# Performance work log

Measured on AMD Instinct MI355X. Metric: run time of the kernel, lower is better.

Reference implementation:

```python
import jax, jax.numpy as jnp
import numpy as np

K = 40        # nearest neighbors
BN_EPS = 1e-5  # nn.BatchNorm1d default eps


def _bn(x, g, b):
    # training-mode BatchNorm1d: batch mean, biased variance
    mu = x.mean(0)
    var = x.var(0)
    return g * (x - mu) / jnp.sqrt(var + BN_EPS) + b


def setup_inputs() -> dict:
    key = jax.random.key(0)
    ks = jax.random.split(key, 16)
    N, Cin, D, S, P = 8192, 16, 32, 3, 32

    def w(k, i, o):
        return jax.random.normal(k, (i, o), jnp.float32) * (1.0 / np.sqrt(i))

    return {
        "x": jax.random.normal(ks[0], (N, Cin), jnp.float32),
        "original_coords": jax.random.normal(ks[1], (N, 3), jnp.float32),
        "batch": jnp.zeros((N,), jnp.int32),
        "step_count": 0,
        "num_layer": 1,
        # pre_gravnet MLP
        "pre_w1": w(ks[2], Cin, D), "pre_b1": jnp.zeros((D,), jnp.float32),
        "pre_w2": w(ks[3], D, D), "pre_b2": jnp.zeros((D,), jnp.float32),
        "bn1_g": jnp.ones((D,), jnp.float32), "bn1_b": jnp.zeros((D,), jnp.float32),
        # GravNetConv projections
        "lin_s_w": w(ks[4], D, S),
        "lin_h_w": w(ks[5], D, P), "lin_h_b": jnp.zeros((P,), jnp.float32),
        "lin_w": w(ks[6], D + 2 * P, D), "lin_b": jnp.zeros((D,), jnp.float32),
        # post_gravnet MLP (in = out_channels + space_dims + d_shape = 32+3+32)
        "post_w1": w(ks[7], D + S + D, D), "post_b1": jnp.zeros((D,), jnp.float32),
        "post_w2": w(ks[8], D, D), "post_b2": jnp.zeros((D,), jnp.float32),
        "bn2_g": jnp.ones((D,), jnp.float32), "bn2_b": jnp.zeros((D,), jnp.float32),
    }


def reference(x, original_coords, batch, step_count, num_layer,
              pre_w1, pre_b1, pre_w2, pre_b2, bn1_g, bn1_b,
              lin_s_w, lin_h_w, lin_h_b, lin_w, lin_b,
              post_w1, post_b1, post_w2, post_b2, bn2_g, bn2_b):
    N = x.shape[0]

    # pre_gravnet MLP + batchnorm
    h = jax.nn.elu(x @ pre_w1 + pre_b1)
    h = jax.nn.elu(h @ pre_w2 + pre_b2)
    x_in = _bn(h, bn1_g, bn1_b)

    # GravNetConv projections
    h_l = x_in @ lin_h_w + lin_h_b          # [N, P] propagated features
    s_l = x_in @ lin_s_w                    # [N, S] learned coordinate space

    # kNN graph in s-space (self loops excluded)
    sq = jnp.sum(s_l * s_l, axis=1)
    d2 = sq[:, None] + sq[None, :] - 2.0 * (s_l @ s_l.T)   # [N, N]
    d2 = jnp.maximum(d2, 0.0)
    d2 = jnp.where(jnp.eye(N, dtype=bool), jnp.inf, d2)
    _, idx = jax.lax.top_k(-d2, K)           # [N, K] neighbor indices

    # per-edge squared distance (NOTE: propagate uses the SQUARED distance,
    # faithful to the source where edge_weight is never re-bound to sqrt)
    edge_sq = jnp.take_along_axis(d2, idx, axis=1)    # [N, K]
    dist = jnp.sqrt(edge_sq + 1e-6)                   # [N, K]

    # DGL-side reductions at dst = edge_index[1] = neighbor index
    dst = idx.reshape(-1)
    distf = dist.reshape(-1)
    indeg = jax.ops.segment_sum(jnp.ones_like(distf), dst, num_segments=N)
    sum_d = jax.ops.segment_sum(distf, dst, num_segments=N)
    avdist = jnp.where(indeg > 0, sum_d / jnp.maximum(indeg, 1.0), 0.0)
    loss_regularizing_neig = 0.01 * jnp.mean(jnp.square(avdist - 0.5))

    norm_d = distf / (sum_d + 1e-4)[dst]              # EdgeWeightNorm('right')
    # faithful to source bug: '_edge_w_gndist' is set to the NORMALIZED dist,
    # and apply_edges multiplies by the RAW '_edge_w'
    degs2 = jax.ops.segment_sum(norm_d, dst, num_segments=N) + 1e-4
    gn_final = distf / degs2[dst]
    loss_llregulariser = 0.1 * jnp.mean(jnp.square(norm_d - gn_final))

    # message passing: msg = h_l[neighbor] * squared_dist, mean+max over the
    # K neighbors of each source node (regular fan-in -> dense reduce)
    msgs = h_l[idx] * edge_sq[..., None]              # [N, K, P]
    agg = jnp.concatenate([msgs.mean(1), msgs.max(1)], axis=-1)  # [N, 2P]
    xgn = jnp.concatenate([agg, x_in], axis=-1) @ lin_w + lin_b   # [N, 32]

    # post_gravnet MLP + batchnorm
    cat = jnp.concatenate([xgn, s_l, x_in], axis=1)   # [N, 67]
    o = jax.nn.elu(cat @ post_w1 + post_b1)
    o = jax.nn.elu(o @ post_w2 + post_b2)
    out = _bn(o, bn2_g, bn2_b)
    return (out, loss_regularizing_neig, loss_llregulariser)
```

## Files before the change

kernel.cpp:

```cpp
#include <hip/hip_runtime.h>
#include <math.h>

#define NPTS 8192
#define KNN 40
#define DD 32
#define CIN 16
#define RPB 8
#define CAP 96

#define OFF_H      0u
#define OFF_XIN    262144u
#define OFF_HL     524288u
#define OFF_SL     786432u
#define OFF_ESQ    819200u
#define OFF_O      1146880u
#define OFF_IDX    1409024u
#define OFF_SUMD   1736704u
#define OFF_INDEG  1744896u
#define OFF_STATS  1753088u
#define ZERO_FLOATS (8192u + 8192u + 130u * 32u)

#define ST(i) stats[(i) * 32]

__device__ __forceinline__ float elu_f(float x) { return x > 0.f ? x : (expf(x) - 1.f); }

__device__ __forceinline__ float grp_sum32(float v) {
#pragma unroll
    for (int m = 1; m < 32; m <<= 1) v += __shfl_xor(v, m);
    return v;
}

__device__ __forceinline__ unsigned fkey(float x) {
    unsigned b = __float_as_uint(x);
    return b ^ ((unsigned)((int)b >> 31) | 0x80000000u);
}
__device__ __forceinline__ float kinv(unsigned k) {
    unsigned b = (k & 0x80000000u) ? (k ^ 0x80000000u) : ~k;
    return __uint_as_float(b);
}

__device__ __forceinline__ unsigned bisect_kth(unsigned u0, unsigned u1, int kth) {
    unsigned lo = 0u, hi = 0xFFFFFFFFu;
    while (lo < hi) {
        unsigned mid = lo + ((hi - lo) >> 1);
        int cnt = __popcll(__ballot(u0 <= mid)) + __popcll(__ballot(u1 <= mid));
        if (cnt >= kth) hi = mid; else lo = mid + 1;
    }
    return hi;
}

__global__ __launch_bounds__(256) void k_pre(const float* __restrict__ x,
    const float* __restrict__ w1, const float* __restrict__ b1,
    const float* __restrict__ w2, const float* __restrict__ b2,
    float* __restrict__ h, float* __restrict__ stats)
{
    __shared__ float sw1[CIN * DD], sw2[DD * DD], sb1[DD], sb2[DD];
    __shared__ float bufx[RPB][20], buft[RPB][36];
    __shared__ float sstat[2 * DD];
    int tid = threadIdx.x;
    for (int t = tid; t < CIN * DD; t += 256) sw1[t] = w1[t];
    for (int t = tid; t < DD * DD; t += 256) sw2[t] = w2[t];
    if (tid < DD) { sb1[tid] = b1[tid]; sb2[tid] = b2[tid]; }
    if (tid < 2 * DD) sstat[tid] = 0.f;

    int r = tid >> 5, ch = tid & 31;
    int g = blockIdx.x * RPB + r;
    if (ch < CIN) bufx[r][ch] = x[(size_t)g * CIN + ch];
    __syncthreads();

    float acc = sb1[ch];
#pragma unroll
    for (int k4 = 0; k4 < CIN; k4 += 4) {
        float4 v = *(const float4*)&bufx[r][k4];
        acc = fmaf(v.x, sw1[(k4 + 0) * DD + ch], acc);
        acc = fmaf(v.y, sw1[(k4 + 1) * DD + ch], acc);
        acc = fmaf(v.z, sw1[(k4 + 2) * DD + ch], acc);
        acc = fmaf(v.w, sw1[(k4 + 3) * DD + ch], acc);
    }
    acc = elu_f(acc);
    buft[r][ch] = acc;
    __syncthreads();

    float o = sb2[ch];
#pragma unroll
    for (int k4 = 0; k4 < DD; k4 += 4) {
        float4 v = *(const float4*)&buft[r][k4];
        o = fmaf(v.x, sw2[(k4 + 0) * DD + ch], o);
        o = fmaf(v.y, sw2[(k4 + 1) * DD + ch], o);
        o = fmaf(v.z, sw2[(k4 + 2) * DD + ch], o);
        o = fmaf(v.w, sw2[(k4 + 3) * DD + ch], o);
    }
    o = elu_f(o);
    h[(size_t)g * DD + ch] = o;

    float s = o + __shfl_xor(o, 32);
    float q = o * o;
    q += __shfl_xor(q, 32);
    if ((tid & 32) == 0) { atomicAdd(&sstat[ch], s); atomicAdd(&sstat[DD + ch], q); }
    __syncthreads();
    if (tid < 2 * DD) atomicAdd(&ST(tid), sstat[tid]);
}

__global__ __launch_bounds__(256) void k_proj(const float* __restrict__ h,
    const float* __restrict__ stats,
    const float* __restrict__ g1, const float* __restrict__ b1g,
    const float* __restrict__ hw, const float* __restrict__ hb,
    const float* __restrict__ sw,
    float* __restrict__ xin, float* __restrict__ hl, float4* __restrict__ sl4)
{
    __shared__ float shw[DD * DD], ssw[DD * 3], sa[DD], sbp[DD], shb[DD];
    __shared__ float rrow[RPB][36];
    int tid = threadIdx.x;
    for (int t = tid; t < DD * DD; t += 256) shw[t] = hw[t];
    if (tid < DD * 3) ssw[tid] = sw[tid];
    if (tid < DD) {
        float mean = ST(tid) * (1.f / NPTS);
        float var = ST(32 + tid) * (1.f / NPTS) - mean * mean;
        float a = g1[tid] * rsqrtf(var + 1e-5f);
        sa[tid] = a;
        sbp[tid] = b1g[tid] - a * mean;
        shb[tid] = hb[tid];
    }
    __syncthreads();

    int r = tid >> 5, ch = tid & 31;
    int g = blockIdx.x * RPB + r;

    float v = fmaf(sa[ch], h[(size_t)g * DD + ch], sbp[ch]);
    xin[(size_t)g * DD + ch] = v;
    rrow[r][ch] = v;

    float p0 = v * ssw[ch * 3 + 0];
    float p1 = v * ssw[ch * 3 + 1];
    float p2 = v * ssw[ch * 3 + 2];
    p0 = grp_sum32(p0); p1 = grp_sum32(p1); p2 = grp_sum32(p2);
    if (ch == 0) sl4[g] = make_float4(p0, p1, p2, 0.5f * (p0 * p0 + p1 * p1 + p2 * p2));
    __syncthreads();

    float o = shb[ch];
#pragma unroll
    for (int k4 = 0; k4 < DD; k4 += 4) {
        float4 vv = *(const float4*)&rrow[r][k4];
        o = fmaf(vv.x, shw[(k4 + 0) * DD + ch], o);
        o = fmaf(vv.y, shw[(k4 + 1) * DD + ch], o);
        o = fmaf(vv.z, shw[(k4 + 2) * DD + ch], o);
        o = fmaf(vv.w, shw[(k4 + 3) * DD + ch], o);
    }
    hl[(size_t)g * DD + ch] = o;
}

__device__ __forceinline__ void select_emit(const float2* bufq, int C, int qidx,
    float qw, int lane, int* __restrict__ idxo, float* __restrict__ esq,
    float* __restrict__ sumd, float* __restrict__ indeg)
{
    float e0 = INFINITY, e1 = INFINITY;
    int j0 = -1, j1 = -1;
    if (lane < C) { float2 t = bufq[lane]; e0 = t.x; j0 = __float_as_int(t.y); }
    if (lane + 64 < C) { float2 t = bufq[lane + 64]; e1 = t.x; j1 = __float_as_int(t.y); }
    if (j0 == qidx) e0 = INFINITY;
    if (j1 == qidx) e1 = INFINITY;
    unsigned u0 = fkey(e0), u1 = fkey(e1);
    unsigned thr = bisect_kth(u0, u1, KNN);
    unsigned long long ltm = (1ull << lane) - 1;
    unsigned long long mlt0 = __ballot(u0 < thr), mlt1 = __ballot(u1 < thr);
    unsigned long long meq0 = __ballot(u0 == thr), meq1 = __ballot(u1 == thr);
    int nlt = __popcll(mlt0) + __popcll(mlt1);
    int need = KNN - nlt;
    int rb = qidx * KNN;

    int pos = -1;
    if (u0 < thr) pos = __popcll(mlt0 & ltm);
    else if (u0 == thr) { int rk = __popcll(meq0 & ltm); if (rk < need) pos = nlt + rk; }
    if (pos >= 0) {
        float d2 = fmaxf(2.f * (e0 + qw), 0.f);
        idxo[rb + pos] = j0; esq[rb + pos] = d2;
        float dist = sqrtf(d2 + 1e-6f);
        atomicAdd(&sumd[j0], dist); atomicAdd(&indeg[j0], 1.f);
    }
    pos = -1;
    if (u1 < thr) pos = __popcll(mlt0) + __popcll(mlt1 & ltm);
    else if (u1 == thr) {
        int rk = __popcll(meq0) + __popcll(meq1 & ltm);
        if (rk < need) pos = nlt + rk;
    }
    if (pos >= 0) {
        float d2 = fmaxf(2.f * (e1 + qw), 0.f);
        idxo[rb + pos] = j1; esq[rb + pos] = d2;
        float dist = sqrtf(d2 + 1e-6f);
        atomicAdd(&sumd[j1], dist); atomicAdd(&indeg[j1], 1.f);
    }
}

__global__ __launch_bounds__(256) void k_knn(const float4* __restrict__ sl4,
    int* __restrict__ idxo, float* __restrict__ esq,
    float* __restrict__ sumd, float* __restrict__ indeg)
{
    __shared__ float2 buf[8][CAP];
    int tid = threadIdx.x, lane = tid & 63, wid = tid >> 6;
    int qai = blockIdx.x * 8 + wid * 2;
    int qbi = qai + 1;
    float4 qa = sl4[qai], qb = sl4[qbi];

    float m0a = INFINITY, m1a = INFINITY, m0b = INFINITY, m1b = INFINITY;
    for (int base = 0; base < NPTS; base += 64) {
        float4 p = sl4[base + lane];
        float ea = fmaf(-qa.x, p.x, fmaf(-qa.y, p.y, fmaf(-qa.z, p.z, p.w)));
        float eb = fmaf(-qb.x, p.x, fmaf(-qb.y, p.y, fmaf(-qb.z, p.z, p.w)));
        float lo = fminf(ea, m0a), hi = fmaxf(ea, m0a);
        m0a = lo; m1a = fminf(m1a, hi);
        lo = fminf(eb, m0b); hi = fmaxf(eb, m0b);
        m0b = lo; m1b = fminf(m1b, hi);
    }
    float thrfa = kinv(bisect_kth(fkey(m0a), fkey(m1a), KNN + 1));
    float thrfb = kinv(bisect_kth(fkey(m0b), fkey(m1b), KNN + 1));

    unsigned long long ltm = (1ull << lane) - 1;
    int ca = 0, cbn = 0;
    float2* bufa = buf[wid * 2];
    float2* bufb = buf[wid * 2 + 1];
    for (int base = 0; base < NPTS; base += 64) {
        float4 p = sl4[base + lane];
        int jj = base + lane;
        float ea = fmaf(-qa.x, p.x, fmaf(-qa.y, p.y, fmaf(-qa.z, p.z, p.w)));
        float eb = fmaf(-qb.x, p.x, fmaf(-qb.y, p.y, fmaf(-qb.z, p.z, p.w)));
        unsigned long long ma = __ballot(ea <= thrfa);
        unsigned long long mb = __ballot(eb <= thrfb);
        if (ma) {
            if (ea <= thrfa) {
                int pos = ca + __popcll(ma & ltm);
                if (pos < CAP) bufa[pos] = make_float2(ea, __int_as_float(jj));
            }
            ca += __popcll(ma);
        }
        if (mb) {
            if (eb <= thrfb) {
                int pos = cbn + __popcll(mb & ltm);
                if (pos < CAP) bufb[pos] = make_float2(eb, __int_as_float(jj));
            }
            cbn += __popcll(mb);
        }
    }
    __syncthreads();

    select_emit(bufa, ca < CAP ? ca : CAP, qai, qa.w, lane, idxo, esq, sumd, indeg);
    select_emit(bufb, cbn < CAP ? cbn : CAP, qbi, qb.w, lane, idxo, esq, sumd, indeg);
}

__global__ __launch_bounds__(256) void k_agg(
    const int* __restrict__ idx, const float* __restrict__ esq,
    const float* __restrict__ hl, const float* __restrict__ xin,
    const float4* __restrict__ sl4,
    const float* __restrict__ sumd, const float* __restrict__ indeg,
    const float* __restrict__ lw, const float* __restrict__ lb,
    const float* __restrict__ pw1, const float* __restrict__ pb1,
    const float* __restrict__ pw2, const float* __restrict__ pb2,
    float* __restrict__ o, float* __restrict__ stats)
{
    __shared__ float slw[96 * DD], spw1[67 * DD], spw2[DD * DD];
    __shared__ float slb[DD], spb1[DD], spb2[DD];
    __shared__ float rbuf[RPB][100];
    __shared__ float rb2[RPB][68];
    __shared__ float sstat[2 * DD];
    __shared__ float sl1, sl2;
    int tid = threadIdx.x;
    for (int t = tid; t < 96 * DD; t += 256) slw[t] = lw[t];
    for (int t = tid; t < 67 * DD; t += 256) spw1[t] = pw1[t];
    for (int t = tid; t < DD * DD; t += 256) spw2[t] = pw2[t];
    if (tid < DD) { slb[tid] = lb[tid]; spb1[tid] = pb1[tid]; spb2[tid] = pb2[tid]; }
    if (tid < 2 * DD) sstat[tid] = 0.f;
    if (tid == 254) sl1 = 0.f;
    if (tid == 255) sl2 = 0.f;

    int r = tid >> 5, ch = tid & 31;
    int g = blockIdx.x * RPB + r;
    int rb = g * KNN;

    float sv = 0.f, mv = -INFINITY;
#pragma unroll 8
    for (int k = 0; k < KNN; ++k) {
        int j = idx[rb + k];
        float w = esq[rb + k];
        float m = hl[(size_t)j * DD + ch] * w;
        sv += m;
        mv = fmaxf(mv, m);
    }
    rbuf[r][ch] = sv * (1.f / KNN);
    rbuf[r][32 + ch] = mv;
    rbuf[r][64 + ch] = xin[(size_t)g * DD + ch];
    if (ch == 0) { float4 s = sl4[g]; rbuf[r][96] = s.x; rbuf[r][97] = s.y; rbuf[r][98] = s.z; }
    __syncthreads();

    float l2 = 0.f;
    {
        int j = idx[rb + ch];
        float w = esq[rb + ch];
        float dist = sqrtf(w + 1e-6f);
        float sd = sumd[j];
        float r1 = 1.f / (sd + 1e-4f);
        float dg = sd * r1 + 1e-4f;
        float df = dist * r1 - dist / dg;
        l2 = df * df;
        if (ch < KNN - 32) {
            j = idx[rb + 32 + ch];
            w = esq[rb + 32 + ch];
            dist = sqrtf(w + 1e-6f);
            sd = sumd[j];
            r1 = 1.f / (sd + 1e-4f);
            dg = sd * r1 + 1e-4f;
            df = dist * r1 - dist / dg;
            l2 += df * df;
        }
    }
    l2 = grp_sum32(l2);
    if (ch == 0) {
        float id = indeg[g], sdg = sumd[g];
        float av = id > 0.f ? sdg / fmaxf(id, 1.f) : 0.f;
        float dd = av - 0.5f;
        atomicAdd(&sl2, l2);
        atomicAdd(&sl1, dd * dd);
    }

    float acc = slb[ch];
#pragma unroll
    for (int k4 = 0; k4 < 96; k4 += 4) {
        float4 v = *(const float4*)&rbuf[r][k4];
        acc = fmaf(v.x, slw[(k4 + 0) * DD + ch], acc);
        acc = fmaf(v.y, slw[(k4 + 1) * DD + ch], acc);
        acc = fmaf(v.z, slw[(k4 + 2) * DD + ch], acc);
        acc = fmaf(v.w, slw[(k4 + 3) * DD + ch], acc);
    }
    rb2[r][ch] = acc;
    __syncthreads();

    acc = spb1[ch];
#pragma unroll
    for (int k4 = 0; k4 < DD; k4 += 4) {
        float4 v = *(const float4*)&rb2[r][k4];
        acc = fmaf(v.x, spw1[(k4 + 0) * DD + ch], acc);
        acc = fmaf(v.y, spw1[(k4 + 1) * DD + ch], acc);
        acc = fmaf(v.z, spw1[(k4 + 2) * DD + ch], acc);
        acc = fmaf(v.w, spw1[(k4 + 3) * DD + ch], acc);
    }
#pragma unroll
    for (int s2 = 0; s2 < 3; ++s2)
        acc = fmaf(rbuf[r][96 + s2], spw1[(32 + s2) * DD + ch], acc);
#pragma unroll
    for (int k4 = 0; k4 < DD; k4 += 4) {
        float4 v = *(const float4*)&rbuf[r][64 + k4];
        acc = fmaf(v.x, spw1[(35 + k4 + 0) * DD + ch], acc);
        acc = fmaf(v.y, spw1[(35 + k4 + 1) * DD + ch], acc);
        acc = fmaf(v.z, spw1[(35 + k4 + 2) * DD + ch], acc);
        acc = fmaf(v.w, spw1[(35 + k4 + 3) * DD + ch], acc);
    }
    acc = elu_f(acc);
    rb2[r][32 + ch] = acc;
    __syncthreads();

    acc = spb2[ch];
#pragma unroll
    for (int k4 = 0; k4 < DD; k4 += 4) {
        float4 v = *(const float4*)&rb2[r][32 + k4];
        acc = fmaf(v.x, spw2[(k4 + 0) * DD + ch], acc);
        acc = fmaf(v.y, spw2[(k4 + 1) * DD + ch], acc);
        acc = fmaf(v.z, spw2[(k4 + 2) * DD + ch], acc);
        acc = fmaf(v.w, spw2[(k4 + 3) * DD + ch], acc);
    }
    acc = elu_f(acc);
    o[(size_t)g * DD + ch] = acc;

    float s = acc + __shfl_xor(acc, 32);
    float q = acc * acc;
    q += __shfl_xor(q, 32);
    if ((tid & 32) == 0) { atomicAdd(&sstat[ch], s); atomicAdd(&sstat[DD + ch], q); }
    __syncthreads();
    if (tid < 2 * DD) atomicAdd(&ST(64 + tid), sstat[tid]);
    if (tid == 0) { atomicAdd(&ST(128), sl1); atomicAdd(&ST(129), sl2); }
}

__global__ __launch_bounds__(256) void k_out(const float* __restrict__ o,
    const float* __restrict__ stats, const float* __restrict__ g,
    const float* __restrict__ b, float* __restrict__ dout)
{
    __shared__ float sa[DD], sb[DD];
    int tid = threadIdx.x;
    if (tid < DD) {
        float mean = ST(64 + tid) * (1.f / NPTS);
        float var = ST(96 + tid) * (1.f / NPTS) - mean * mean;
        float a = g[tid] * rsqrtf(var + 1e-5f);
        sa[tid] = a;
        sb[tid] = b[tid] - a * mean;
    }
    __syncthreads();

    int t = blockIdx.x * 256 + tid;
    float4 v = ((const float4*)o)[t];
    int cbase = (t * 4) & (DD - 1);
    float4 rr;
    rr.x = fmaf(sa[cbase + 0], v.x, sb[cbase + 0]);
    rr.y = fmaf(sa[cbase + 1], v.y, sb[cbase + 1]);
    rr.z = fmaf(sa[cbase + 2], v.z, sb[cbase + 2]);
    rr.w = fmaf(sa[cbase + 3], v.w, sb[cbase + 3]);
    ((float4*)dout)[t] = rr;

    if (blockIdx.x == 0) {
        if (tid == DD)     dout[NPTS * DD]     = 0.01f * ST(128) * (1.f / NPTS);
        if (tid == DD + 1) dout[NPTS * DD + 1] = 0.1f  * ST(129) * (1.f / ((float)NPTS * KNN));
    }
}

extern "C" void kernel_launch(void* const* d_in, const int* in_sizes, int n_in,
                              void* d_out, int out_size, void* d_ws, size_t ws_size,
                              hipStream_t stream)
{
    (void)in_sizes; (void)n_in; (void)out_size; (void)ws_size;
    const float* x      = (const float*)d_in[0];
    const float* pre_w1 = (const float*)d_in[5];
    const float* pre_b1 = (const float*)d_in[6];
    const float* pre_w2 = (const float*)d_in[7];
    const float* pre_b2 = (const float*)d_in[8];
    const float* bn1_g  = (const float*)d_in[9];
    const float* bn1_b  = (const float*)d_in[10];
    const float* lin_s_w = (const float*)d_in[11];
    const float* lin_h_w = (const float*)d_in[12];
    const float* lin_h_b = (const float*)d_in[13];
    const float* lin_w   = (const float*)d_in[14];
    const float* lin_b   = (const float*)d_in[15];
    const float* post_w1 = (const float*)d_in[16];
    const float* post_b1 = (const float*)d_in[17];
    const float* post_w2 = (const float*)d_in[18];
    const float* post_b2 = (const float*)d_in[19];
    const float* bn2_g   = (const float*)d_in[20];
    const float* bn2_b   = (const float*)d_in[21];

    float* W = (float*)d_ws;
    float* h     = W + OFF_H;
    float* xin   = W + OFF_XIN;
    float* hl    = W + OFF_HL;
    float4* sl4  = (float4*)(W + OFF_SL);
    float* esq   = W + OFF_ESQ;
    float* o     = W + OFF_O;
    int*   idx   = (int*)(W + OFF_IDX);
    float* sumd  = W + OFF_SUMD;
    float* indeg = W + OFF_INDEG;
    float* stats = W + OFF_STATS;
    float* dout  = (float*)d_out;

    hipMemsetAsync(W + OFF_SUMD, 0, ZERO_FLOATS * sizeof(float), stream);

    k_pre<<<NPTS / RPB, 256, 0, stream>>>(x, pre_w1, pre_b1, pre_w2, pre_b2, h, stats);
    k_proj<<<NPTS / RPB, 256, 0, stream>>>(h, stats, bn1_g, bn1_b,
                                           lin_h_w, lin_h_b, lin_s_w, xin, hl, sl4);
    k_knn<<<NPTS / 8, 256, 0, stream>>>(sl4, idx, esq, sumd, indeg);
    k_agg<<<NPTS / RPB, 256, 0, stream>>>(idx, esq, hl, xin, sl4, sumd, indeg,
                                          lin_w, lin_b, post_w1, post_b1, post_w2, post_b2,
                                          o, stats);
    k_out<<<NPTS * DD / 1024, 256, 0, stream>>>(o, stats, bn2_g, bn2_b, dout);
}
```

Baseline: 131.9 us.

## Stage kNN candidate points through double-buffered shared-memory tiles

The kNN kernel's two scan passes now cooperatively load 1024-point tiles of the s-space coordinates into LDS with register prefetch of the next tile, instead of each wave streaming all points from global memory. The aim is to cut redundant global/L2 traffic, since each of the four waves in a block currently reads the full point set twice. It adds block-wide barriers per tile and 32 KB of extra LDS, which may lower occupancy. The data is already small and L2-resident, so the gain depends on whether the scan is bound by memory or by ALU work.

Result: slower. 138.9 us (+5.3%).

```diff
diff --git a/kernel.cpp b/kernel.cpp
--- a/kernel.cpp
+++ b/kernel.cpp
@@ -7,6 +7,8 @@
 #define CIN 16
 #define RPB 8
 #define CAP 96
+#define TILE4 1024
+#define NT (NPTS / TILE4)
 
 #define OFF_H      0u
 #define OFF_XIN    262144u
@@ -191,59 +193,107 @@
     }
 }
 
+#define EDIST(p, qq) fmaf(-(qq).x, (p).x, fmaf(-(qq).y, (p).y, fmaf(-(qq).z, (p).z, (p).w)))
+#define TOP2Q(pt, qq, m0, m1) { \
+        float e = EDIST(pt, qq); \
+        float lo = fminf(e, m0), hi = fmaxf(e, m0); \
+        m0 = lo; m1 = fminf(m1, hi); }
+
 __global__ __launch_bounds__(256) void k_knn(const float4* __restrict__ sl4,
     int* __restrict__ idxo, float* __restrict__ esq,
     float* __restrict__ sumd, float* __restrict__ indeg)
 {
-    __shared__ float2 buf[8][CAP];
-    int tid = threadIdx.x, lane = tid & 63, wid = tid >> 6;
-    int qai = blockIdx.x * 8 + wid * 2;
-    int qbi = qai + 1;
+    __shared__ float4 tile[2][TILE4];
+    __shared__ float2 cand[8][CAP];
+    int tid = threadIdx.x, lane = tid & 63, w = tid >> 6;
+    int qbase = blockIdx.x * 8;
+    int qai = qbase + 2 * w, qbi = qai + 1;
     float4 qa = sl4[qai], qb = sl4[qbi];
+    int sbase = w * 256 + lane;
 
     float m0a = INFINITY, m1a = INFINITY, m0b = INFINITY, m1b = INFINITY;
-    for (int base = 0; base < NPTS; base += 64) {
-        float4 p = sl4[base + lane];
-        float ea = fmaf(-qa.x, p.x, fmaf(-qa.y, p.y, fmaf(-qa.z, p.z, p.w)));
-        float eb = fmaf(-qb.x, p.x, fmaf(-qb.y, p.y, fmaf(-qb.z, p.z, p.w)));
-        float lo = fminf(ea, m0a), hi = fmaxf(ea, m0a);
-        m0a = lo; m1a = fminf(m1a, hi);
-        lo = fminf(eb, m0b); hi = fmaxf(eb, m0b);
-        m0b = lo; m1b = fminf(m1b, hi);
+    tile[0][sbase]       = sl4[sbase];
+    tile[0][sbase + 64]  = sl4[sbase + 64];
+    tile[0][sbase + 128] = sl4[sbase + 128];
+    tile[0][sbase + 192] = sl4[sbase + 192];
+    __syncthreads();
+    int cur = 0;
+    for (int t = 0; t < NT; ++t) {
+        float4 r0, r1, r2, r3;
+        bool more = (t + 1 < NT);
+        if (more) {
+            int nb = (t + 1) * TILE4 + sbase;
+            r0 = sl4[nb]; r1 = sl4[nb + 64]; r2 = sl4[nb + 128]; r3 = sl4[nb + 192];
+        }
+        const float4* tp = tile[cur];
+#pragma unroll 4
+        for (int i = 0; i < TILE4 / 64; ++i) {
+            float4 p = tp[i * 64 + lane];
+            TOP2Q(p, qa, m0a, m1a)
+            TOP2Q(p, qb, m0b, m1b)
+        }
+        if (more) {
+            tile[cur ^ 1][sbase] = r0;
+            tile[cur ^ 1][sbase + 64] = r1;
+            tile[cur ^ 1][sbase + 128] = r2;
+            tile[cur ^ 1][sbase + 192] = r3;
+        }
+        __syncthreads();
+        if (more) cur ^= 1;
     }
     float thrfa = kinv(bisect_kth(fkey(m0a), fkey(m1a), KNN + 1));
     float thrfb = kinv(bisect_kth(fkey(m0b), fkey(m1b), KNN + 1));
 
     unsigned long long ltm = (1ull << lane) - 1;
-    int ca = 0, cbn = 0;
-    float2* bufa = buf[wid * 2];
-    float2* bufb = buf[wid * 2 + 1];
-    for (int base = 0; base < NPTS; base += 64) {
-        float4 p = sl4[base + lane];
-        int jj = base + lane;
-        float ea = fmaf(-qa.x, p.x, fmaf(-qa.y, p.y, fmaf(-qa.z, p.z, p.w)));
-        float eb = fmaf(-qb.x, p.x, fmaf(-qb.y, p.y, fmaf(-qb.z, p.z, p.w)));
-        unsigned long long ma = __ballot(ea <= thrfa);
-        unsigned long long mb = __ballot(eb <= thrfb);
-        if (ma) {
-            if (ea <= thrfa) {
-                int pos = ca + __popcll(ma & ltm);
-                if (pos < CAP) bufa[pos] = make_float2(ea, __int_as_float(jj));
-            }
-            ca += __popcll(ma);
-        }
-        if (mb) {
-            if (eb <= thrfb) {
-                int pos = cbn + __popcll(mb & ltm);
-                if (pos < CAP) bufb[pos] = make_float2(eb, __int_as_float(jj));
-            }
-            cbn += __popcll(mb);
-        }
-    }
-    __syncthreads();
+    int ca = 0, cb = 0;
+    float2* bufa = cand[2 * w];
+    float2* bufb = cand[2 * w + 1];
+
+#define COLL(e, thrv, cnt, brow, jj) { \
+        unsigned long long mm = __ballot((e) <= (thrv)); \
+        if (mm) { \
+            if ((e) <= (thrv)) { \
+                int pos = cnt + __popcll(mm & ltm); \
+                if (pos < CAP) brow[pos] = make_float2((e), __int_as_float(jj)); \
+            } \
+            cnt += __popcll(mm); \
+        } }
+
+    tile[0][sbase]       = sl4[sbase];
+    tile[0][sbase + 64]  = sl4[sbase + 64];
+    tile[0][sbase + 128] = sl4[sbase + 128];
+    tile[0][sbase + 192] = sl4[sbase + 192];
+    __syncthreads();
+    cur = 0;
+    for (int t = 0; t < NT; ++t) {
+        float4 r0, r1, r2, r3;
+        bool more = (t + 1 < NT);
+        if (more) {
+            int nb = (t + 1) * TILE4 + sbase;
+            r0 = sl4[nb]; r1 = sl4[nb + 64]; r2 = sl4[nb + 128]; r3 = sl4[nb + 192];
+        }
+        const float4* tp = tile[cur];
+        int tb = t * TILE4;
+#pragma unroll 4
+        for (int i = 0; i < TILE4 / 64; ++i) {
+            float4 p = tp[i * 64 + lane];
+            int jj = tb + i * 64 + lane;
+            float ea = EDIST(p, qa), eb = EDIST(p, qb);
+            COLL(ea, thrfa, ca, bufa, jj)
+            COLL(eb, thrfb, cb, bufb, jj)
+        }
+        if (more) {
+            tile[cur ^ 1][sbase] = r0;
+            tile[cur ^ 1][sbase + 64] = r1;
+            tile[cur ^ 1][sbase + 128] = r2;
+            tile[cur ^ 1][sbase + 192] = r3;
+        }
+        __syncthreads();
+        if (more) cur ^= 1;
+    }
 
     select_emit(bufa, ca < CAP ? ca : CAP, qai, qa.w, lane, idxo, esq, sumd, indeg);
-    select_emit(bufb, cbn < CAP ? cbn : CAP, qbi, qb.w, lane, idxo, esq, sumd, indeg);
+    select_emit(bufb, cb < CAP ? cb : CAP, qbi, qb.w, lane, idxo, esq, sumd, indeg);
 }
 
 __global__ __launch_bounds__(256) void k_agg(
```

## Stage kNN candidate points through double-buffered LDS tiles with async global-to-LDS loads

Applied to the files above, without the earlier changes.

The kNN kernel now launches 512-thread blocks handling 16 queries. It streams the point coordinates in 2048-point tiles into double-buffered shared memory using global_load_lds, so both passes read points from LDS instead of each wave re-reading global memory. Query coordinates are made wave-uniform with readfirstlane so they can live in scalar registers. The cost is 64 KB of LDS tiles plus block-wide barriers per tile, which may limit occupancy.

New measurement: 120.6 us (median of 2 runs). 8.6% less time.

```diff
diff --git a/kernel.cpp b/kernel.cpp
--- a/kernel.cpp
+++ b/kernel.cpp
@@ -6,6 +6,9 @@
 #define DD 32
 #define CIN 16
 #define RPB 8
+#define QT 2048
+#define NQTR 4
+#define KQPB 16
 #define CAP 96
 
 #define OFF_H      0u
@@ -28,6 +31,10 @@
 #pragma unroll
     for (int m = 1; m < 32; m <<= 1) v += __shfl_xor(v, m);
     return v;
+}
+
+__device__ __forceinline__ float rfl(float v) {
+    return __int_as_float(__builtin_amdgcn_readfirstlane(__float_as_int(v)));
 }
 
 __device__ __forceinline__ unsigned fkey(float x) {
@@ -191,59 +198,89 @@
     }
 }
 
-__global__ __launch_bounds__(256) void k_knn(const float4* __restrict__ sl4,
+typedef __attribute__((address_space(1))) const unsigned glds_src_t;
+typedef __attribute__((address_space(3))) unsigned glds_dst_t;
+
+__global__ __launch_bounds__(512, 4) void k_knn(const float4* __restrict__ sl4,
     int* __restrict__ idxo, float* __restrict__ esq,
     float* __restrict__ sumd, float* __restrict__ indeg)
 {
-    __shared__ float2 buf[8][CAP];
-    int tid = threadIdx.x, lane = tid & 63, wid = tid >> 6;
-    int qai = blockIdx.x * 8 + wid * 2;
-    int qbi = qai + 1;
-    float4 qa = sl4[qai], qb = sl4[qbi];
+    __shared__ float4 tile[2][QT];
+    __shared__ float2 cand[KQPB][CAP];
+    int tid = threadIdx.x, lane = tid & 63, w = tid >> 6;
+    int qbase = blockIdx.x * KQPB;
+    int qai = qbase + 2 * w, qbi = qai + 1;
+    float4 qa4 = sl4[qai], qb4 = sl4[qbi];
+    float qax = rfl(qa4.x), qay = rfl(qa4.y), qaz = rfl(qa4.z);
+    float qbx = rfl(qb4.x), qby = rfl(qb4.y), qbz = rfl(qb4.z);
+
+#define STAGE(qt, b) { \
+    _Pragma("unroll") \
+    for (int c = 0; c < 4; ++c) { \
+        int off = w * 256 + c * 64; \
+        __builtin_amdgcn_global_load_lds( \
+            (glds_src_t*)(sl4 + (qt) * QT + off + lane), \
+            (glds_dst_t*)&tile[b][off], 16, 0, 0); \
+    } }
+
+#define EDQ(p, ex, ey, ez) fmaf(-(ex), (p).x, fmaf(-(ey), (p).y, fmaf(-(ez), (p).z, (p).w)))
 
     float m0a = INFINITY, m1a = INFINITY, m0b = INFINITY, m1b = INFINITY;
-    for (int base = 0; base < NPTS; base += 64) {
-        float4 p = sl4[base + lane];
-        float ea = fmaf(-qa.x, p.x, fmaf(-qa.y, p.y, fmaf(-qa.z, p.z, p.w)));
-        float eb = fmaf(-qb.x, p.x, fmaf(-qb.y, p.y, fmaf(-qb.z, p.z, p.w)));
-        float lo = fminf(ea, m0a), hi = fmaxf(ea, m0a);
-        m0a = lo; m1a = fminf(m1a, hi);
-        lo = fminf(eb, m0b); hi = fmaxf(eb, m0b);
-        m0b = lo; m1b = fminf(m1b, hi);
-    }
-    float thrfa = kinv(bisect_kth(fkey(m0a), fkey(m1a), KNN + 1));
-    float thrfb = kinv(bisect_kth(fkey(m0b), fkey(m1b), KNN + 1));
+    STAGE(0, 0)
+    __syncthreads();
+    for (int t = 0; t < NQTR; ++t) {
+        if (t + 1 < NQTR) STAGE(t + 1, (t + 1) & 1)
+        const float4* tp = tile[t & 1];
+#pragma unroll 4
+        for (int i = 0; i < QT / 64; ++i) {
+            float4 p = tp[i * 64 + lane];
+            float ea = EDQ(p, qax, qay, qaz);
+            float eb = EDQ(p, qbx, qby, qbz);
+            float lo = fminf(ea, m0a), hi = fmaxf(ea, m0a);
+            m0a = lo; m1a = fminf(m1a, hi);
+            lo = fminf(eb, m0b); hi = fmaxf(eb, m0b);
+            m0b = lo; m1b = fminf(m1b, hi);
+        }
+        __syncthreads();
+    }
+    float thra = kinv(bisect_kth(fkey(m0a), fkey(m1a), KNN + 1));
+    float thrb = kinv(bisect_kth(fkey(m0b), fkey(m1b), KNN + 1));
 
     unsigned long long ltm = (1ull << lane) - 1;
-    int ca = 0, cbn = 0;
-    float2* bufa = buf[wid * 2];
-    float2* bufb = buf[wid * 2 + 1];
-    for (int base = 0; base < NPTS; base += 64) {
-        float4 p = sl4[base + lane];
-        int jj = base + lane;
-        float ea = fmaf(-qa.x, p.x, fmaf(-qa.y, p.y, fmaf(-qa.z, p.z, p.w)));
-        float eb = fmaf(-qb.x, p.x, fmaf(-qb.y, p.y, fmaf(-qb.z, p.z, p.w)));
-        unsigned long long ma = __ballot(ea <= thrfa);
-        unsigned long long mb = __ballot(eb <= thrfb);
-        if (ma) {
-            if (ea <= thrfa) {
-                int pos = ca + __popcll(ma & ltm);
-                if (pos < CAP) bufa[pos] = make_float2(ea, __int_as_float(jj));
-            }
-            ca += __popcll(ma);
+    int ca = 0, cb = 0;
+    float2* bufa = cand[2 * w];
+    float2* bufb = cand[2 * w + 1];
+
+#define COLL(e, thrv, cnt, brow, jj) { \
+        unsigned long long mm = __ballot((e) <= (thrv)); \
+        if (mm) { \
+            if ((e) <= (thrv)) { \
+                int pos = cnt + __popcll(mm & ltm); \
+                if (pos < CAP) brow[pos] = make_float2((e), __int_as_float(jj)); \
+            } \
+            cnt += __popcll(mm); \
+        } }
+
+    STAGE(0, 0)
+    __syncthreads();
+    for (int t = 0; t < NQTR; ++t) {
+        if (t + 1 < NQTR) STAGE(t + 1, (t + 1) & 1)
+        const float4* tp = tile[t & 1];
+        int tb = t * QT;
+#pragma unroll 4
+        for (int i = 0; i < QT / 64; ++i) {
+            float4 p = tp[i * 64 + lane];
+            int jj = tb + i * 64 + lane;
+            float ea = EDQ(p, qax, qay, qaz);
+            float eb = EDQ(p, qbx, qby, qbz);
+            COLL(ea, thra, ca, bufa, jj)
+            COLL(eb, thrb, cb, bufb, jj)
         }
-        if (mb) {
-            if (eb <= thrfb) {
-                int pos = cbn + __popcll(mb & ltm);
-                if (pos < CAP) bufb[pos] = make_float2(eb, __int_as_float(jj));
-            }
-            cbn += __popcll(mb);
-        }
-    }
-    __syncthreads();
-
-    select_emit(bufa, ca < CAP ? ca : CAP, qai, qa.w, lane, idxo, esq, sumd, indeg);
-    select_emit(bufb, cbn < CAP ? cbn : CAP, qbi, qb.w, lane, idxo, esq, sumd, indeg);
+        __syncthreads();
+    }
+
+    select_emit(bufa, ca < CAP ? ca : CAP, qai, rfl(qa4.w), lane, idxo, esq, sumd, indeg);
+    select_emit(bufb, cb < CAP ? cb : CAP, qbi, rfl(qb4.w), lane, idxo, esq, sumd, indeg);
 }
 
 __global__ __launch_bounds__(256) void k_agg(
@@ -450,7 +487,7 @@
     k_pre<<<NPTS / RPB, 256, 0, stream>>>(x, pre_w1, pre_b1, pre_w2, pre_b2, h, stats);
     k_proj<<<NPTS / RPB, 256, 0, stream>>>(h, stats, bn1_g, bn1_b,
                                            lin_h_w, lin_h_b, lin_s_w, xin, hl, sl4);
-    k_knn<<<NPTS / 8, 256, 0, stream>>>(sl4, idx, esq, sumd, indeg);
+    k_knn<<<NPTS / KQPB, 512, 0, stream>>>(sl4, idx, esq, sumd, indeg);
     k_agg<<<NPTS / RPB, 256, 0, stream>>>(idx, esq, hl, xin, sl4, sumd, indeg,
                                           lin_w, lin_b, post_w1, post_b1, post_w2, post_b2,
                                           o, stats);
```
